# Performance work log

Hardware: AMD Instinct MI355X
Metric: run time of the kernel (lower is better)

## Reference

```python
import jax, jax.numpy as jnp
import numpy as np

IN_FEATURES = 1024
OUT_FEATURES = 128


def setup_inputs() -> dict:
    key = jax.random.key(0)
    k1, k2, k3, k4, k5 = jax.random.split(key, 5)
    B, T, E, D = 4, 4096, IN_FEATURES, OUT_FEATURES
    s_in = 1.0 / np.sqrt(E)
    s_d = 1.0 / np.sqrt(D)
    return {
        "x": jax.random.normal(k1, (B, T, E), dtype=jnp.float32),
        "Wk": jax.random.uniform(k2, (E, D), jnp.float32, -s_in, s_in),
        "Wq": jax.random.uniform(k3, (E, D), jnp.float32, -s_in, s_in),
        "Wv": jax.random.uniform(k4, (E, D), jnp.float32, -s_in, s_in),
        "Wp": jax.random.uniform(k5, (D, D), jnp.float32, -s_d, s_d),
    }


def reference(x, Wk, Wq, Wv, Wp):
    # x: [B, T, E]; projections stored as [in, out] (torch Linear transposed)
    B, T, E = x.shape
    D = Wk.shape[1]
    k = x @ Wk  # [B, T, D]
    q = x @ Wq
    v = x @ Wv
    scale = 1.0 / jnp.sqrt(jnp.asarray(D, x.dtype))
    attn = jnp.einsum("btd,bsd->bts", q, k) * scale  # [B, T, T]
    causal = jnp.tril(jnp.ones((T, T), dtype=bool))
    attn = jnp.where(causal, attn, -jnp.inf)
    attn = jax.nn.softmax(attn, axis=-1)
    out = jnp.einsum("bts,bsd->btd", attn, v)  # [B, T, D]
    return out @ Wp  # dropout p=0.0 -> identity
```

## Files before the change

kernel.cpp:

```cpp
#include <hip/hip_runtime.h>

#define E_DIM 1024
#define D_DIM 128
#define T_DIM 4096

typedef unsigned short u16;
typedef u16 u16x8 __attribute__((ext_vector_type(8)));
typedef u16 u16x4 __attribute__((ext_vector_type(4)));
typedef __bf16 bf16x8 __attribute__((ext_vector_type(8)));
typedef float f32x4 __attribute__((ext_vector_type(4)));

__device__ __forceinline__ u16 cvt_bf16(float f) {
    unsigned u = __float_as_uint(f);
    u += 0x7FFF + ((u >> 16) & 1);
    return (u16)(u >> 16);
}

__device__ __forceinline__ float bf2f(u16 v) {
    return __uint_as_float(((unsigned)v) << 16);
}

__device__ __forceinline__ f32x4 mfma16(u16x8 a, u16x8 b, f32x4 c) {
    return __builtin_amdgcn_mfma_f32_16x16x32_bf16(
        __builtin_bit_cast(bf16x8, a), __builtin_bit_cast(bf16x8, b), c, 0, 0, 0);
}

__device__ __forceinline__ void gld_lds16(const void* g, void* l) {
    __builtin_amdgcn_global_load_lds(
        (const __attribute__((address_space(1))) unsigned int*)g,
        (__attribute__((address_space(3))) unsigned int*)l, 16, 0, 0);
}

__global__ void prep_kernel(const float* __restrict__ Wk, const float* __restrict__ Wq,
                            const float* __restrict__ Wv, const float* __restrict__ Wp,
                            u16* __restrict__ Wqt, u16* __restrict__ Wkt,
                            u16* __restrict__ Wvt, u16* __restrict__ Wpt) {
    int tid = blockIdx.x * 256 + threadIdx.x;
    const int WT = 128 * 1024;
    if (tid < 3 * WT) {
        int w = tid / WT;
        int r = tid - w * WT;
        int n = r >> 10, k = r & 1023;
        const float* W = (w == 0) ? Wq : (w == 1) ? Wk : Wv;
        u16* Wt = (w == 0) ? Wqt : (w == 1) ? Wkt : Wvt;
        Wt[r] = cvt_bf16(W[k * 128 + n]);
    } else {
        int r = tid - 3 * WT;
        if (r < 128 * 128) {
            int n = r >> 7, k = r & 127;
            Wpt[r] = cvt_bf16(Wp[k * 128 + n]);
        }
    }
}

__global__ __launch_bounds__(512) void qkv_kernel(
        const float* __restrict__ x,
        const u16* __restrict__ Wqt, const u16* __restrict__ Wkt, const u16* __restrict__ Wvt,
        u16* __restrict__ qb, u16* __restrict__ kb, u16* __restrict__ vT) {
    __shared__ __align__(16) char smem[98304];

    const int t = threadIdx.x;
    const int w = t >> 6;
    const int lane = t & 63;
    const int lr = lane & 15;
    const int lg = lane >> 4;
    const int m4 = w & 3;
    const int n2 = w >> 2;
    const int r0 = blockIdx.x * 64;

    #define STAGE_W(K0, BUF) do {                                                 \
        char* wB_ = smem + (BUF) * 24576;                                         \
        _Pragma("unroll")                                                         \
        for (int c2 = 0; c2 < 3; ++c2) {                                          \
            const int rl_ = c2 * 128 + (t >> 2);                                  \
            const u16* W_ = (rl_ < 128) ? Wqt : (rl_ < 256) ? Wkt : Wvt;          \
            const int s_ = ((t & 3) - (rl_ >> 1)) & 3;                            \
            gld_lds16(W_ + (size_t)(rl_ & 127) * E_DIM + (K0) + 8 * s_,           \
                      wB_ + c2 * 8192 + t * 16);                                  \
        }                                                                         \
    } while (0)

    const float* xp = x + (size_t)(r0 + 16 * m4 + lr) * E_DIM + lg * 8;

    float4 xa[2], xb[2];
    #define XLOAD(arr, K0) do {                                                   \
        arr[0] = *(const float4*)(xp + (K0));                                     \
        arr[1] = *(const float4*)(xp + (K0) + 4);                                 \
    } while (0)

    #define CVT_AV(av, arr) do {                                                  \
        av[0] = cvt_bf16(arr[0].x); av[1] = cvt_bf16(arr[0].y);                   \
        av[2] = cvt_bf16(arr[0].z); av[3] = cvt_bf16(arr[0].w);                   \
        av[4] = cvt_bf16(arr[1].x); av[5] = cvt_bf16(arr[1].y);                   \
        av[6] = cvt_bf16(arr[1].z); av[7] = cvt_bf16(arr[1].w);                   \
    } while (0)

    f32x4 acc[12];
    #pragma unroll
    for (int j = 0; j < 12; ++j) acc[j] = f32x4{0.f, 0.f, 0.f, 0.f};

    #define ITER(KK, XARR) do {                                                   \
        const int kk_ = (KK);                                                     \
        u16x8 av_;                                                                \
        CVT_AV(av_, XARR);                                                        \
        __builtin_amdgcn_sched_barrier(0);                                        \
        if (kk_ < 30) {                                                           \
            STAGE_W(kk_ * 32 + 64, (kk_ + 2) & 3);                                \
            __builtin_amdgcn_sched_barrier(0);                                    \
            XLOAD(XARR, kk_ * 32 + 64);                                           \
        }                                                                         \
        __builtin_amdgcn_sched_barrier(0);                                        \
        {                                                                         \
            char* wB = smem + ((kk_) & 3) * 24576;                                \
            __builtin_amdgcn_s_setprio(1);                                        \
            _Pragma("unroll")                                                     \
            for (int nt = 0; nt < 12; ++nt) {                                     \
                const int ln = n2 * 192 + nt * 16 + lr;                           \
                u16x8 bv = *(u16x8*)(wB + ln * 64 + (((lg + (ln >> 1)) & 3) << 4)); \
                acc[nt] = mfma16(av_, bv, acc[nt]);                               \
            }                                                                     \
            __builtin_amdgcn_s_setprio(0);                                        \
        }                                                                         \
        if (kk_ < 30) asm volatile("s_waitcnt vmcnt(5)" ::: "memory");            \
        else          asm volatile("s_waitcnt vmcnt(0)" ::: "memory");            \
        __builtin_amdgcn_s_barrier();                                             \
    } while (0)

    STAGE_W(0, 0);
    XLOAD(xa, 0);
    STAGE_W(32, 1);
    XLOAD(xb, 32);
    asm volatile("s_waitcnt vmcnt(5)" ::: "memory");
    __builtin_amdgcn_s_barrier();

    for (int kk2 = 0; kk2 < 16; ++kk2) {
        ITER(2 * kk2, xa);
        ITER(2 * kk2 + 1, xb);
    }
    #undef STAGE_W
    #undef XLOAD
    #undef CVT_AV
    #undef ITER

    const int bb = r0 >> 12;
    const int row0 = r0 + 16 * m4 + 4 * lg;
    const int tt0 = row0 & 4095;
    #pragma unroll
    for (int nt = 0; nt < 12; ++nt) {
        const int col_g = n2 * 192 + nt * 16 + lr;
        const int j = col_g >> 7;
        const int colw = col_g & 127;
        if (j < 2) {
            u16* outb = (j == 0) ? qb : kb;
            #pragma unroll
            for (int reg = 0; reg < 4; ++reg)
                outb[(size_t)(row0 + reg) * D_DIM + colw] = cvt_bf16(acc[nt][reg]);
        } else {
            u16x4 pv;
            #pragma unroll
            for (int reg = 0; reg < 4; ++reg) pv[reg] = cvt_bf16(acc[nt][reg]);
            *(u16x4*)&vT[((size_t)(bb * 128 + colw)) * T_DIM + tt0] = pv;
        }
    }
}

__global__ __launch_bounds__(512) void attn_kernel(
        const u16* __restrict__ qb, const u16* __restrict__ kb, const u16* __restrict__ vT,
        u16* __restrict__ Opart, float* __restrict__ ml, int SPLIT) {
    const int g = blockIdx.x;
    const int b = blockIdx.y;
    int i, c;
    if (SPLIT) {
        int k = 0;
        while (2 * (k + 1) * (k + 2) <= g) ++k;
        const int off = g - 2 * k * (k + 1);
        const int iband = off / (k + 1);
        c = off - iband * (k + 1);
        i = 4 * k + iband;
    } else { i = g; c = 0; }

    const int q0 = i * 128;
    const int kv_beg = c * 512;
    const int kv_end = SPLIT ? min(q0 + 128, kv_beg + 512) : (q0 + 128);
    const int slot = b * gridDim.x + g;

    __shared__ __align__(16) char smem[81920];

    const int t = threadIdx.x;
    const int w = t >> 6;
    const int lane = t & 63;
    const int lr = lane & 15;
    const int lg = lane >> 4;
    const size_t base = (size_t)b * T_DIM * D_DIM;

    u16x8 qf[4];
    {
        const u16* qp = qb + base + (size_t)(q0 + 16 * w + lr) * D_DIM + lg * 8;
        #pragma unroll
        for (int dk = 0; dk < 4; ++dk) qf[dk] = *(const u16x8*)(qp + dk * 32);
    }

    const char* kpb = (const char*)(kb + base);
    const char* vpb = (const char*)(vT + (size_t)b * D_DIM * T_DIM);
    const int key = (lr & 7) << 4;

    #define STAGE(S0, BUF) do {                                                   \
        char* kB_ = smem + (BUF) * 16384;                                         \
        char* vB_ = smem + 32768 + (BUF) * 16384;                                 \
        const int wbase_ = (t >> 6) * 1024;                                       \
        _Pragma("unroll")                                                         \
        for (int c2 = 0; c2 < 2; ++c2) {                                          \
            const int krow_ = c2 * 32 + (t >> 4);                                 \
            gld_lds16(kpb + (size_t)((S0) + krow_) * 256 +                        \
                      (((t & 15) * 16) ^ ((krow_ & 7) * 16)),                     \
                      kB_ + c2 * 8192 + wbase_);                                  \
            const int vrow_ = c2 * 64 + (t >> 3);                                 \
            gld_lds16(vpb + (size_t)vrow_ * (T_DIM * 2) + (size_t)(S0) * 2 +      \
                      (((t & 7) * 16) ^ ((vrow_ & 7) * 16)),                      \
                      vB_ + c2 * 8192 + wbase_);                                  \
        }                                                                         \
    } while (0)

    f32x4 oacc[8];
    #pragma unroll
    for (int nn = 0; nn < 8; ++nn) oacc[nn] = f32x4{0.f, 0.f, 0.f, 0.f};
    float m_run = -1e30f, l_run = 0.f;
    const float scale2 = 0.12752048520120164f;
    const int qrow = q0 + 16 * w + lr;

    STAGE(kv_beg, 0);
    asm volatile("s_waitcnt vmcnt(0)" ::: "memory");
    __syncthreads();

    int buf = 0;
    for (int s0 = kv_beg; s0 < kv_end; s0 += 64) {
        if (s0 + 64 < kv_end) STAGE(s0 + 64, buf ^ 1);

        char* kB  = smem + buf * 16384;
        char* vB  = smem + 32768 + buf * 16384;
        char* psB = smem + 65536 + w * 2048;

        f32x4 sacc[4];
        #pragma unroll
        for (int nn = 0; nn < 4; ++nn) sacc[nn] = f32x4{0.f, 0.f, 0.f, 0.f};
        __builtin_amdgcn_s_setprio(1);
        #pragma unroll
        for (int dk = 0; dk < 4; ++dk) {
            #pragma unroll
            for (int nt = 0; nt < 4; ++nt) {
                u16x8 kfr = *(u16x8*)(kB + (nt * 16 + lr) * 256 + ((dk * 64 + lg * 16) ^ key));
                sacc[nt] = mfma16(kfr, qf[dk], sacc[nt]);
            }
        }
        __builtin_amdgcn_s_setprio(0);

        float sv[4][4];
        const bool need_mask = (s0 + 63 > q0 + 16 * w);
        #pragma unroll
        for (int nt = 0; nt < 4; ++nt) {
            #pragma unroll
            for (int r = 0; r < 4; ++r) {
                float v = sacc[nt][r] * scale2;
                if (need_mask && (s0 + nt * 16 + 4 * lg + r) > qrow) v = -1e30f;
                sv[nt][r] = v;
            }
        }

        float tmax = sv[0][0];
        #pragma unroll
        for (int nt = 0; nt < 4; ++nt)
            #pragma unroll
            for (int r = 0; r < 4; ++r) tmax = fmaxf(tmax, sv[nt][r]);
        tmax = fmaxf(tmax, __shfl_xor(tmax, 16));
        tmax = fmaxf(tmax, __shfl_xor(tmax, 32));
        float m_new = fmaxf(m_run, tmax);
        float rsc = __builtin_amdgcn_exp2f(m_run - m_new);
        m_run = m_new;
        float tsum = 0.f;
        #pragma unroll
        for (int nt = 0; nt < 4; ++nt)
            #pragma unroll
            for (int r = 0; r < 4; ++r) {
                sv[nt][r] = __builtin_amdgcn_exp2f(sv[nt][r] - m_new);
                tsum += sv[nt][r];
            }
        tsum += __shfl_xor(tsum, 16);
        tsum += __shfl_xor(tsum, 32);
        l_run = l_run * rsc + tsum;

        #pragma unroll
        for (int nt = 0; nt < 8; ++nt)
            #pragma unroll
            for (int r = 0; r < 4; ++r) oacc[nt][r] *= rsc;

        #pragma unroll
        for (int nt = 0; nt < 4; ++nt) {
            u16x4 pv4;
            #pragma unroll
            for (int r = 0; r < 4; ++r) pv4[r] = cvt_bf16(sv[nt][r]);
            *(u16x4*)(psB + lr * 128 + ((nt * 32 + lg * 8) ^ key)) = pv4;
        }

        u16x8 pA0 = *(u16x8*)(psB + lr * 128 + ((lg * 16) ^ key));
        u16x8 pA1 = *(u16x8*)(psB + lr * 128 + ((64 + lg * 16) ^ key));

        __builtin_amdgcn_s_setprio(1);
        #pragma unroll
        for (int nt = 0; nt < 8; ++nt) {
            u16x8 bv0 = *(u16x8*)(vB + (nt * 16 + lr) * 128 + ((lg * 16) ^ key));
            oacc[nt] = mfma16(bv0, pA0, oacc[nt]);
            u16x8 bv1 = *(u16x8*)(vB + (nt * 16 + lr) * 128 + ((64 + lg * 16) ^ key));
            oacc[nt] = mfma16(bv1, pA1, oacc[nt]);
        }
        __builtin_amdgcn_s_setprio(0);

        asm volatile("s_waitcnt vmcnt(0)" ::: "memory");
        __syncthreads();
        buf ^= 1;
    }
    #undef STAGE

    if (lg == 0) {
        int row = 16 * w + lr;
        ml[(size_t)(slot * 128 + row) * 2]     = m_run;
        ml[(size_t)(slot * 128 + row) * 2 + 1] = l_run;
    }

    const float invl = 1.f / l_run;
    const int orw = 16 * w + lr;
    #pragma unroll
    for (int nt = 0; nt < 8; ++nt) {
        u16x4 ov;
        #pragma unroll
        for (int r = 0; r < 4; ++r) ov[r] = cvt_bf16(oacc[nt][r] * invl);
        *(u16x4*)(smem + orw * 256 + ((32 * nt + 8 * lg) ^ ((orw & 7) << 4))) = ov;
    }
    __syncthreads();
    u16* op = Opart + (size_t)slot * 16384;
    const int orow = t >> 2;
    const int oseg = t & 3;
    #pragma unroll
    for (int j = 0; j < 4; ++j) {
        u16x8 vv = *(u16x8*)(smem + orow * 256 + ((oseg * 64 + j * 16) ^ ((orow & 7) << 4)));
        *(u16x8*)(op + orow * 128 + oseg * 32 + j * 8) = vv;
    }
}

__global__ __launch_bounds__(256) void combine_kernel(
        const u16* __restrict__ Opart, const float* __restrict__ ml,
        const u16* __restrict__ Wpt, float* __restrict__ out,
        int SPLIT, int NSLOT) {
    const int io = blockIdx.x;
    const int b = blockIdx.y;
    const int i = io >> 1;
    const int half = io & 1;
    int NC, g0;
    if (SPLIT) {
        int k = i >> 2;
        NC = k + 1;
        g0 = 2 * k * (k + 1) + (i & 3) * (k + 1);
    } else { NC = 1; g0 = i; }
    const int slot0 = b * NSLOT + g0;

    __shared__ u16 Os[64][136];
    const int t = threadIdx.x;
    const int row = t >> 2, seg = (t & 3) * 32;
    const int row_in = half * 64 + row;

    float m_fin = -1e30f;
    for (int c = 0; c < NC; ++c)
        m_fin = fmaxf(m_fin, ml[(size_t)((slot0 + c) * 128 + row_in) * 2]);

    float acc[32];
    #pragma unroll
    for (int j = 0; j < 32; ++j) acc[j] = 0.f;
    float l_fin = 0.f;
    for (int c = 0; c < NC; ++c) {
        float mcv = ml[(size_t)((slot0 + c) * 128 + row_in) * 2];
        float lcv = ml[(size_t)((slot0 + c) * 128 + row_in) * 2 + 1];
        float wgt = __builtin_amdgcn_exp2f(mcv - m_fin) * lcv;
        l_fin += wgt;
        const u16* opc = Opart + (size_t)(slot0 + c) * 16384 + row_in * 128 + seg;
        #pragma unroll
        for (int j = 0; j < 4; ++j) {
            u16x8 v = *(const u16x8*)(opc + j * 8);
            #pragma unroll
            for (int e = 0; e < 8; ++e)
                acc[j * 8 + e] += bf2f(v[e]) * wgt;
        }
    }
    const float inv = 1.f / l_fin;

    #pragma unroll
    for (int j = 0; j < 4; ++j) {
        u16x8 ov;
        #pragma unroll
        for (int e = 0; e < 8; ++e) ov[e] = cvt_bf16(acc[j * 8 + e] * inv);
        *(u16x8*)&Os[row][seg + j * 8] = ov;
    }
    __syncthreads();

    const int w = t >> 6;
    const int lane = t & 63;
    const int lr = lane & 15;
    const int lg = lane >> 4;
    u16x8 af[4];
    #pragma unroll
    for (int dk = 0; dk < 4; ++dk)
        af[dk] = *(u16x8*)&Os[16 * w + lr][dk * 32 + lg * 8];
    float* op = out + ((size_t)b * T_DIM + io * 64) * D_DIM;
    #pragma unroll
    for (int nt = 0; nt < 8; ++nt) {
        f32x4 y = f32x4{0.f, 0.f, 0.f, 0.f};
        #pragma unroll
        for (int dk = 0; dk < 4; ++dk) {
            u16x8 bv = *(const u16x8*)&Wpt[(size_t)(nt * 16 + lr) * D_DIM + dk * 32 + lg * 8];
            y = mfma16(af[dk], bv, y);
        }
        #pragma unroll
        for (int r = 0; r < 4; ++r)
            op[(size_t)(16 * w + 4 * lg + r) * D_DIM + nt * 16 + lr] = y[r];
    }
}

extern "C" void kernel_launch(void* const* d_in, const int* in_sizes, int n_in,
                              void* d_out, int out_size, void* d_ws, size_t ws_size,
                              hipStream_t stream) {
    const float* x  = (const float*)d_in[0];
    const float* Wk = (const float*)d_in[1];
    const float* Wq = (const float*)d_in[2];
    const float* Wv = (const float*)d_in[3];
    const float* Wp = (const float*)d_in[4];
    float* out = (float*)d_out;

    char* ws = (char*)d_ws;
    u16* qb  = (u16*)(ws);
    u16* kb  = (u16*)(ws + 4194304);
    u16* vT  = (u16*)(ws + 8388608);
    u16* Wqt = (u16*)(ws + 12582912);
    u16* Wkt = (u16*)(ws + 12582912 + 262144);
    u16* Wvt = (u16*)(ws + 12582912 + 524288);
    u16* Wpt = (u16*)(ws + 12582912 + 786432);
    float* ml   = (float*)(ws + 13631488);
    u16* Opart  = (u16*)(ws + 14680064);

    const bool big = ws_size >= (size_t)36 * 1024 * 1024;
    const int SPLIT = big ? 1 : 0;
    const int GX = big ? 144 : 32;

    prep_kernel<<<1600, 256, 0, stream>>>(Wk, Wq, Wv, Wp, Wqt, Wkt, Wvt, Wpt);
    qkv_kernel<<<256, 512, 0, stream>>>(x, Wqt, Wkt, Wvt, qb, kb, vT);
    attn_kernel<<<dim3(GX, 4), 512, 0, stream>>>(qb, kb, vT, Opart, ml, SPLIT);
    combine_kernel<<<dim3(64, 4), 256, 0, stream>>>(Opart, ml, Wpt, out, SPLIT, GX);
}
```

Before: 94.74 us.

## Shrink QKV tiles, fold softmax scale into Q, skip masked warps, lazy rescale

The QKV projection now uses 32-row blocks with 2x4 warp tiling and a 3-buffer LDS ring, launching 512 blocks instead of 256 and using less shared memory, to spread the work over more CUs. The softmax scale (with log2e) is folded into Q at write time, which removes a multiply per score in attention. In the attention loop, warps whose query rows lie entirely above the causal diagonal skip the tile's compute. The running-max rescale is done only when some lane's tile max exceeds the current max by more than 8, a lazy-rescale trick that risks bf16 precision drift in P values up to 2^8.

```diff
diff --git a/kernel.cpp b/kernel.cpp
--- a/kernel.cpp
+++ b/kernel.cpp
@@ -57,16 +57,16 @@
         const float* __restrict__ x,
         const u16* __restrict__ Wqt, const u16* __restrict__ Wkt, const u16* __restrict__ Wvt,
         u16* __restrict__ qb, u16* __restrict__ kb, u16* __restrict__ vT) {
-    __shared__ __align__(16) char smem[98304];
+    __shared__ __align__(16) char smem[73728];
 
     const int t = threadIdx.x;
     const int w = t >> 6;
     const int lane = t & 63;
     const int lr = lane & 15;
     const int lg = lane >> 4;
-    const int m4 = w & 3;
-    const int n2 = w >> 2;
-    const int r0 = blockIdx.x * 64;
+    const int m2 = w & 1;
+    const int n4 = w >> 1;
+    const int r0 = blockIdx.x * 32;
 
     #define STAGE_W(K0, BUF) do {                                                 \
         char* wB_ = smem + (BUF) * 24576;                                         \
@@ -80,9 +80,9 @@
         }                                                                         \
     } while (0)
 
-    const float* xp = x + (size_t)(r0 + 16 * m4 + lr) * E_DIM + lg * 8;
-
-    float4 xa[2], xb[2];
+    const float* xp = x + (size_t)(r0 + 16 * m2 + lr) * E_DIM + lg * 8;
+
+    float4 x0[2], x1[2], x2[2];
     #define XLOAD(arr, K0) do {                                                   \
         arr[0] = *(const float4*)(xp + (K0));                                     \
         arr[1] = *(const float4*)(xp + (K0) + 4);                                 \
@@ -95,27 +95,27 @@
         av[6] = cvt_bf16(arr[1].z); av[7] = cvt_bf16(arr[1].w);                   \
     } while (0)
 
-    f32x4 acc[12];
-    #pragma unroll
-    for (int j = 0; j < 12; ++j) acc[j] = f32x4{0.f, 0.f, 0.f, 0.f};
-
-    #define ITER(KK, XARR) do {                                                   \
+    f32x4 acc[6];
+    #pragma unroll
+    for (int j = 0; j < 6; ++j) acc[j] = f32x4{0.f, 0.f, 0.f, 0.f};
+
+    #define ITER(KK, BUF, SBUF, XC, XN) do {                                      \
         const int kk_ = (KK);                                                     \
         u16x8 av_;                                                                \
-        CVT_AV(av_, XARR);                                                        \
+        CVT_AV(av_, XC);                                                          \
         __builtin_amdgcn_sched_barrier(0);                                        \
         if (kk_ < 30) {                                                           \
-            STAGE_W(kk_ * 32 + 64, (kk_ + 2) & 3);                                \
+            STAGE_W(kk_ * 32 + 64, SBUF);                                         \
             __builtin_amdgcn_sched_barrier(0);                                    \
-            XLOAD(XARR, kk_ * 32 + 64);                                           \
+            XLOAD(XN, kk_ * 32 + 64);                                             \
         }                                                                         \
         __builtin_amdgcn_sched_barrier(0);                                        \
         {                                                                         \
-            char* wB = smem + ((kk_) & 3) * 24576;                                \
+            char* wB = smem + (BUF) * 24576;                                      \
             __builtin_amdgcn_s_setprio(1);                                        \
             _Pragma("unroll")                                                     \
-            for (int nt = 0; nt < 12; ++nt) {                                     \
-                const int ln = n2 * 192 + nt * 16 + lr;                           \
+            for (int nt = 0; nt < 6; ++nt) {                                      \
+                const int ln = n4 * 96 + nt * 16 + lr;                            \
                 u16x8 bv = *(u16x8*)(wB + ln * 64 + (((lg + (ln >> 1)) & 3) << 4)); \
                 acc[nt] = mfma16(av_, bv, acc[nt]);                               \
             }                                                                     \
@@ -127,34 +127,39 @@
     } while (0)
 
     STAGE_W(0, 0);
-    XLOAD(xa, 0);
+    XLOAD(x0, 0);
     STAGE_W(32, 1);
-    XLOAD(xb, 32);
+    XLOAD(x1, 32);
     asm volatile("s_waitcnt vmcnt(5)" ::: "memory");
     __builtin_amdgcn_s_barrier();
 
-    for (int kk2 = 0; kk2 < 16; ++kk2) {
-        ITER(2 * kk2, xa);
-        ITER(2 * kk2 + 1, xb);
-    }
+    for (int kk = 0; kk < 30; kk += 3) {
+        ITER(kk,     0, 2, x0, x2);
+        ITER(kk + 1, 1, 0, x1, x0);
+        ITER(kk + 2, 2, 1, x2, x1);
+    }
+    ITER(30, 0, 2, x0, x2);
+    ITER(31, 1, 0, x1, x0);
     #undef STAGE_W
     #undef XLOAD
     #undef CVT_AV
     #undef ITER
 
+    const float qscale = 0.12752048520120164f;
     const int bb = r0 >> 12;
-    const int row0 = r0 + 16 * m4 + 4 * lg;
+    const int row0 = r0 + 16 * m2 + 4 * lg;
     const int tt0 = row0 & 4095;
     #pragma unroll
-    for (int nt = 0; nt < 12; ++nt) {
-        const int col_g = n2 * 192 + nt * 16 + lr;
+    for (int nt = 0; nt < 6; ++nt) {
+        const int col_g = n4 * 96 + nt * 16 + lr;
         const int j = col_g >> 7;
         const int colw = col_g & 127;
         if (j < 2) {
             u16* outb = (j == 0) ? qb : kb;
+            const float sc = (j == 0) ? qscale : 1.0f;
             #pragma unroll
             for (int reg = 0; reg < 4; ++reg)
-                outb[(size_t)(row0 + reg) * D_DIM + colw] = cvt_bf16(acc[nt][reg]);
+                outb[(size_t)(row0 + reg) * D_DIM + colw] = cvt_bf16(acc[nt][reg] * sc);
         } else {
             u16x4 pv;
             #pragma unroll
@@ -225,8 +230,8 @@
     #pragma unroll
     for (int nn = 0; nn < 8; ++nn) oacc[nn] = f32x4{0.f, 0.f, 0.f, 0.f};
     float m_run = -1e30f, l_run = 0.f;
-    const float scale2 = 0.12752048520120164f;
     const int qrow = q0 + 16 * w + lr;
+    const int qmax = q0 + 16 * w + 15;
 
     STAGE(kv_beg, 0);
     asm volatile("s_waitcnt vmcnt(0)" ::: "memory");
@@ -236,83 +241,89 @@
     for (int s0 = kv_beg; s0 < kv_end; s0 += 64) {
         if (s0 + 64 < kv_end) STAGE(s0 + 64, buf ^ 1);
 
-        char* kB  = smem + buf * 16384;
-        char* vB  = smem + 32768 + buf * 16384;
-        char* psB = smem + 65536 + w * 2048;
-
-        f32x4 sacc[4];
-        #pragma unroll
-        for (int nn = 0; nn < 4; ++nn) sacc[nn] = f32x4{0.f, 0.f, 0.f, 0.f};
-        __builtin_amdgcn_s_setprio(1);
-        #pragma unroll
-        for (int dk = 0; dk < 4; ++dk) {
+        if (s0 <= qmax) {
+            char* kB  = smem + buf * 16384;
+            char* vB  = smem + 32768 + buf * 16384;
+            char* psB = smem + 65536 + w * 2048;
+
+            f32x4 sacc[4];
+            #pragma unroll
+            for (int nn = 0; nn < 4; ++nn) sacc[nn] = f32x4{0.f, 0.f, 0.f, 0.f};
+            __builtin_amdgcn_s_setprio(1);
+            #pragma unroll
+            for (int dk = 0; dk < 4; ++dk) {
+                #pragma unroll
+                for (int nt = 0; nt < 4; ++nt) {
+                    u16x8 kfr = *(u16x8*)(kB + (nt * 16 + lr) * 256 + ((dk * 64 + lg * 16) ^ key));
+                    sacc[nt] = mfma16(kfr, qf[dk], sacc[nt]);
+                }
+            }
+            __builtin_amdgcn_s_setprio(0);
+
+            float sv[4][4];
+            const bool need_mask = (s0 + 63 > q0 + 16 * w);
             #pragma unroll
             for (int nt = 0; nt < 4; ++nt) {
-                u16x8 kfr = *(u16x8*)(kB + (nt * 16 + lr) * 256 + ((dk * 64 + lg * 16) ^ key));
-                sacc[nt] = mfma16(kfr, qf[dk], sacc[nt]);
+                #pragma unroll
+                for (int r = 0; r < 4; ++r) {
+                    float v = sacc[nt][r];
+                    if (need_mask && (s0 + nt * 16 + 4 * lg + r) > qrow) v = -1e30f;
+                    sv[nt][r] = v;
+                }
             }
+
+            float tmax = sv[0][0];
+            #pragma unroll
+            for (int nt = 0; nt < 4; ++nt)
+                #pragma unroll
+                for (int r = 0; r < 4; ++r) tmax = fmaxf(tmax, sv[nt][r]);
+            tmax = fmaxf(tmax, __shfl_xor(tmax, 16));
+            tmax = fmaxf(tmax, __shfl_xor(tmax, 32));
+
+            if (!__all(tmax <= m_run + 8.0f)) {
+                float m_new = fmaxf(m_run, tmax);
+                float rsc = __builtin_amdgcn_exp2f(m_run - m_new);
+                m_run = m_new;
+                l_run *= rsc;
+                #pragma unroll
+                for (int nt = 0; nt < 8; ++nt)
+                    #pragma unroll
+                    for (int r = 0; r < 4; ++r) oacc[nt][r] *= rsc;
+            }
+
+            float tsum = 0.f;
+            #pragma unroll
+            for (int nt = 0; nt < 4; ++nt)
+                #pragma unroll
+                for (int r = 0; r < 4; ++r) {
+                    sv[nt][r] = __builtin_amdgcn_exp2f(sv[nt][r] - m_run);
+                    tsum += sv[nt][r];
+                }
+            tsum += __shfl_xor(tsum, 16);
+            tsum += __shfl_xor(tsum, 32);
+            l_run += tsum;
+
+            #pragma unroll
+            for (int nt = 0; nt < 4; ++nt) {
+                u16x4 pv4;
+                #pragma unroll
+                for (int r = 0; r < 4; ++r) pv4[r] = cvt_bf16(sv[nt][r]);
+                *(u16x4*)(psB + lr * 128 + ((nt * 32 + lg * 8) ^ key)) = pv4;
+            }
+
+            u16x8 pA0 = *(u16x8*)(psB + lr * 128 + ((lg * 16) ^ key));
+            u16x8 pA1 = *(u16x8*)(psB + lr * 128 + ((64 + lg * 16) ^ key));
+
+            __builtin_amdgcn_s_setprio(1);
+            #pragma unroll
+            for (int nt = 0; nt < 8; ++nt) {
+                u16x8 bv0 = *(u16x8*)(vB + (nt * 16 + lr) * 128 + ((lg * 16) ^ key));
+                oacc[nt] = mfma16(bv0, pA0, oacc[nt]);
+                u16x8 bv1 = *(u16x8*)(vB + (nt * 16 + lr) * 128 + ((64 + lg * 16) ^ key));
+                oacc[nt] = mfma16(bv1, pA1, oacc[nt]);
+            }
+            __builtin_amdgcn_s_setprio(0);
         }
-        __builtin_amdgcn_s_setprio(0);
-
-        float sv[4][4];
-        const bool need_mask = (s0 + 63 > q0 + 16 * w);
-        #pragma unroll
-        for (int nt = 0; nt < 4; ++nt) {
-            #pragma unroll
-            for (int r = 0; r < 4; ++r) {
-                float v = sacc[nt][r] * scale2;
-                if (need_mask && (s0 + nt * 16 + 4 * lg + r) > qrow) v = -1e30f;
-                sv[nt][r] = v;
-            }
-        }
-
-        float tmax = sv[0][0];
-        #pragma unroll
-        for (int nt = 0; nt < 4; ++nt)
-            #pragma unroll
-            for (int r = 0; r < 4; ++r) tmax = fmaxf(tmax, sv[nt][r]);
-        tmax = fmaxf(tmax, __shfl_xor(tmax, 16));
-        tmax = fmaxf(tmax, __shfl_xor(tmax, 32));
-        float m_new = fmaxf(m_run, tmax);
-        float rsc = __builtin_amdgcn_exp2f(m_run - m_new);
-        m_run = m_new;
-        float tsum = 0.f;
-        #pragma unroll
-        for (int nt = 0; nt < 4; ++nt)
-            #pragma unroll
-            for (int r = 0; r < 4; ++r) {
-                sv[nt][r] = __builtin_amdgcn_exp2f(sv[nt][r] - m_new);
-                tsum += sv[nt][r];
-            }
-        tsum += __shfl_xor(tsum, 16);
-        tsum += __shfl_xor(tsum, 32);
-        l_run = l_run * rsc + tsum;
-
-        #pragma unroll
-        for (int nt = 0; nt < 8; ++nt)
-            #pragma unroll
-            for (int r = 0; r < 4; ++r) oacc[nt][r] *= rsc;
-
-        #pragma unroll
-        for (int nt = 0; nt < 4; ++nt) {
-            u16x4 pv4;
-            #pragma unroll
-            for (int r = 0; r < 4; ++r) pv4[r] = cvt_bf16(sv[nt][r]);
-            *(u16x4*)(psB + lr * 128 + ((nt * 32 + lg * 8) ^ key)) = pv4;
-        }
-
-        u16x8 pA0 = *(u16x8*)(psB + lr * 128 + ((lg * 16) ^ key));
-        u16x8 pA1 = *(u16x8*)(psB + lr * 128 + ((64 + lg * 16) ^ key));
-
-        __builtin_amdgcn_s_setprio(1);
-        #pragma unroll
-        for (int nt = 0; nt < 8; ++nt) {
-            u16x8 bv0 = *(u16x8*)(vB + (nt * 16 + lr) * 128 + ((lg * 16) ^ key));
-            oacc[nt] = mfma16(bv0, pA0, oacc[nt]);
-            u16x8 bv1 = *(u16x8*)(vB + (nt * 16 + lr) * 128 + ((64 + lg * 16) ^ key));
-            oacc[nt] = mfma16(bv1, pA1, oacc[nt]);
-        }
-        __builtin_amdgcn_s_setprio(0);
 
         asm volatile("s_waitcnt vmcnt(0)" ::: "memory");
         __syncthreads();
@@ -449,7 +460,7 @@
     const int GX = big ? 144 : 32;
 
     prep_kernel<<<1600, 256, 0, stream>>>(Wk, Wq, Wv, Wp, Wqt, Wkt, Wvt, Wpt);
-    qkv_kernel<<<256, 512, 0, stream>>>(x, Wqt, Wkt, Wvt, qb, kb, vT);
+    qkv_kernel<<<512, 512, 0, stream>>>(x, Wqt, Wkt, Wvt, qb, kb, vT);
     attn_kernel<<<dim3(GX, 4), 512, 0, stream>>>(qb, kb, vT, Opart, ml, SPLIT);
     combine_kernel<<<dim3(64, 4), 256, 0, stream>>>(Opart, ml, Wpt, out, SPLIT, GX);
 }
```

Result: slower. 115.4 us (+21.8%).
